# Optimization experiments

Measured on AMD Instinct MI355X. Metric: run time of the kernel, lower is better.

## Reference

```python
import jax, jax.numpy as jnp
import numpy as np

WIRES = 4
LAYERS = 2
FEAT = 16

_CNOT = jnp.array([[1, 0, 0, 0], [0, 1, 0, 0], [0, 0, 0, 1], [0, 0, 1, 0]], dtype=jnp.complex64)


def _ry(t):
    c = jnp.cos(t / 2).astype(jnp.complex64)
    s = jnp.sin(t / 2).astype(jnp.complex64)
    return jnp.stack([jnp.stack([c, -s], -1), jnp.stack([s, c], -1)], -2)


def _rx(t):
    c = jnp.cos(t / 2).astype(jnp.complex64)
    s = (-1j) * jnp.sin(t / 2).astype(jnp.complex64)
    return jnp.stack([jnp.stack([c, s], -1), jnp.stack([s, c], -1)], -2)


def _rz(t):
    e = jnp.exp(-0.5j * t.astype(jnp.complex64))
    z = jnp.zeros_like(e)
    return jnp.stack([jnp.stack([e, z], -1), jnp.stack([z, jnp.conj(e)], -1)], -2)


def _apply1(state, U, q):
    # state: (B, 2,...,2); U: (B,2,2) per-sample or (2,2) shared
    state = jnp.moveaxis(state, 1 + q, -1)
    if U.ndim == 3:
        state = jnp.einsum('b...i,bji->b...j', state, U)
    else:
        state = jnp.einsum('...i,ji->...j', state, U)
    return jnp.moveaxis(state, -1, 1 + q)


def _apply2(state, U, c, t):
    state = jnp.moveaxis(state, (1 + c, 1 + t), (-2, -1))
    shp = state.shape
    state = jnp.einsum('...i,ji->...j', state.reshape(shp[:-2] + (4,)), U).reshape(shp)
    return jnp.moveaxis(state, (-2, -1), (1 + c, 1 + t))


def _circuit(a1, a2, w):
    # a1, a2: (B, WIRES) embedding angles; w: (LAYERS, 3*WIRES) ansatz weights
    B = a1.shape[0]
    state = jnp.zeros((B,) + (2,) * WIRES, jnp.complex64).at[(slice(None),) + (0,) * WIRES].set(1.0)
    for q in range(WIRES):  # AngleEmbedding rotation='Y'
        state = _apply1(state, _ry(a1[:, q]), q)
    for q in range(WIRES):  # AngleEmbedding rotation='Z'
        state = _apply1(state, _rz(a2[:, q]), q)
    for l in range(LAYERS):
        for i in range(WIRES):
            state = _apply2(state, _CNOT, i, (i + 1) % WIRES)
        for i in range(WIRES):
            state = _apply2(state, _CNOT, i, (i + 2) % WIRES)
        for i in range(WIRES):
            state = _apply1(state, _rx(w[l, 3 * i + 0]), i)
            state = _apply1(state, _ry(w[l, 3 * i + 1]), i)
            state = _apply1(state, _rz(w[l, 3 * i + 2]), i)
    probs = state.real ** 2 + state.imag ** 2  # (B, 2,...,2)
    evs = []
    for q in range(WIRES):  # expval of PauliZ on each wire
        p = jnp.moveaxis(probs, 1 + q, 1).reshape(B, 2, -1).sum(-1)
        evs.append(p[:, 0] - p[:, 1])
    return jnp.stack(evs, -1)  # (B, WIRES)


def _qlayer(w, Xf):
    a = Xf[:, :WIRES]  # first `wires` features feed the angle embedding
    return _circuit(jnp.arctan(a), jnp.arctan(a * a), w)


def _forward(x, phi, Wd, bd):
    B, T, F = x.shape

    def step(carry, x_t):
        c, h = carry
        z = jnp.concatenate([x_t, h], -1) @ Wd + bd
        Xf = 2.0 * jax.nn.sigmoid(z) - 1.0
        f = jax.nn.sigmoid(_qlayer(phi[0], Xf))
        i = jax.nn.sigmoid(_qlayer(phi[1], Xf))
        Cg = jax.nn.sigmoid(_qlayer(phi[2], Xf))
        o = jax.nn.sigmoid(_qlayer(phi[3], Xf))
        c_new = f * c + i * Cg
        resc = o * jnp.tanh(c_new)
        h_new = _qlayer(phi[4], resc)
        y = _qlayer(phi[5], resc)
        return (c_new, h_new), y

    step = jax.checkpoint(step)
    c0 = jnp.zeros((B, WIRES), x.dtype)
    (c, h), ys = jax.lax.scan(step, (c0, c0), jnp.swapaxes(x, 0, 1))
    return jnp.swapaxes(ys, 0, 1), c, h  # (B,T,WIRES), (B,WIRES), (B,WIRES)


def setup_inputs() -> dict:
    key = jax.random.key(0)
    k1, k2, k3 = jax.random.split(key, 3)
    B, T, F = 4096, 128, FEAT
    D = F + WIRES
    return {
        'x': jax.random.normal(k1, (B, T, F), jnp.float32),
        'phi': 0.001 * jax.random.normal(k2, (6, LAYERS, 3 * WIRES), jnp.float32),
        'Wd': jax.random.normal(k3, (D, D), jnp.float32) / np.float32(np.sqrt(D)),
        'bd': jnp.zeros((D,), jnp.float32),
    }


def reference(x, phi, Wd, bd):
    return _forward(x, phi, Wd, bd)
```

## Files before the change

kernel.cpp:

```cpp
#include <hip/hip_runtime.h>
#include <math.h>

#define TSTEPS 128
#define NFEAT 16
#define NELEM 16

typedef __fp16 f16;
typedef __fp16 f16x2 __attribute__((ext_vector_type(2)));
typedef __fp16 f16x8 __attribute__((ext_vector_type(8)));
typedef float f32x2 __attribute__((ext_vector_type(2)));
typedef float f32x4 __attribute__((ext_vector_type(4)));

union F8 { f16x8 v; f16x2 h[4]; };

__device__ __forceinline__ float frcp(float x){ return __builtin_amdgcn_rcpf(x); }
__device__ __forceinline__ float frsq(float x){ return __builtin_amdgcn_rsqf(x); }
__device__ __forceinline__ float bperm(int addr, float v){
    return __int_as_float(__builtin_amdgcn_ds_bpermute(addr, __float_as_int(v)));
}
__device__ __forceinline__ f16x2 pkrtz(float a, float b){
    return __builtin_amdgcn_cvt_pkrtz(a, b);
}
__device__ __forceinline__ float dpp_xor1(float v){
    return __int_as_float(__builtin_amdgcn_update_dpp(0, __float_as_int(v), 0xB1, 0xF, 0xF, true));
}
__device__ __forceinline__ float dpp_xor2(float v){
    return __int_as_float(__builtin_amdgcn_update_dpp(0, __float_as_int(v), 0x4E, 0xF, 0xF, true));
}
__device__ __forceinline__ float swz_xor4(float v){
    return __int_as_float(__builtin_amdgcn_ds_swizzle(__float_as_int(v), 0x101F));
}
__device__ __forceinline__ float swz_xor8(float v){
    return __int_as_float(__builtin_amdgcn_ds_swizzle(__float_as_int(v), 0x201F));
}
template<int MASK> __device__ __forceinline__ float pshfl(float v){
    if constexpr (MASK == 1) return dpp_xor1(v);
    else if constexpr (MASK == 2) return dpp_xor2(v);
    else if constexpr (MASK == 4) return swz_xor4(v);
    else return swz_xor8(v);
}
__device__ __forceinline__ void cfence(){ __asm__ __volatile__("" ::: "memory"); }

__device__ __forceinline__ float sigm(float x){ return frcp(1.f + __expf(-x)); }
__device__ __forceinline__ float tanh_f(float x){ return 1.f - 2.f * frcp(__expf(2.f*x) + 1.f); }

__device__ __forceinline__ f32x2 cmul(f32x2 a, f32x2 b){
    f32x2 bs = {b.y, b.x};
    f32x2 ar = {a.x, a.x};
    f32x2 ai = {-a.y, a.y};
    return ar*b + ai*bs;
}

template<int I>
__device__ __forceinline__ void gate_step(float &re, float &im,
                                          const float* gt, int ai, int loff){
    const float4 g = *(const float4*)((const char*)gt + ai + loff);
    float pre = pshfl<(1 << I)>(re);
    float pim = pshfl<(1 << I)>(im);
    float nre = g.x*re - g.y*im + g.z*pre - g.w*pim;
    float nim = g.x*im + g.y*re + g.z*pim + g.w*pre;
    re = nre; im = nim;
}

__device__ __forceinline__ void factors(float u, float &F0r, float &F0i,
                                        float &F1r, float &F1i){
    float u2  = u * u;
    float ca1 = frsq(1.f + u2);
    float ca2 = frsq(1.f + u2*u2);
    float x1  = (1.f + ca1) * 0.5f;
    float x2  = (1.f + ca2) * 0.5f;
    float x12 = x1 * x2;
    float t   = frsq(x12);
    float a1  = u  * ca1 * 0.5f;
    float a2  = u2 * ca2 * 0.5f;
    F0r = x12 * t;
    F0i = -(a2 * x1 * t);
    F1r = a1 * x2 * t;
    F1i = a1 * a2 * t;
}

__device__ __forceinline__ void write_F(float* bc, int e, int s,
                                        float F0r, float F0i, float F1r, float F1i){
    float4 w;
    w.x = F0r; w.y = F0i; w.z = F1r; w.w = F1i;
    *(float4*)(bc + e*20 + s*4) = w;
}

__device__ __forceinline__ void build_psi(const float* bc, int e, int sm1, int sm2,
                                          F8 &bp){
    const float4 w0 = *(const float4*)(bc + e*20);
    const float4 w1 = *(const float4*)(bc + e*20 + 4);
    const f32x2 F2 = *(const f32x2*)(bc + e*20 + 8  + sm1*2);
    const f32x2 F3 = *(const f32x2*)(bc + e*20 + 12 + sm2*2);
    f32x2 w00 = {w0.x, w0.y}, w01 = {w0.z, w0.w};
    f32x2 w10 = {w1.x, w1.y}, w11 = {w1.z, w1.w};
    f32x2 pre = cmul(F2, F3);
    f32x2 P0 = cmul(pre, w10);
    f32x2 P1 = cmul(pre, w11);
    f32x2 a0 = cmul(P0, w00);
    f32x2 a1 = cmul(P0, w01);
    f32x2 a2 = cmul(P1, w00);
    f32x2 a3 = cmul(P1, w01);
    bp.h[0] = pkrtz(a0.x, a0.y);
    bp.h[1] = pkrtz(a1.x, a1.y);
    bp.h[2] = pkrtz(a2.x, a2.y);
    bp.h[3] = pkrtz(a3.x, a3.y);
}

__device__ __forceinline__ F8 pack_P(const f32x4 &reE, const f32x4 &imE,
                                     const f32x4 &reO, const f32x4 &imO){
    f32x4 pE = reE*reE + imE*imE;
    f32x4 pO = reO*reO + imO*imO;
    F8 b;
    b.h[0] = pkrtz(pE[0], pE[1]);
    b.h[1] = pkrtz(pE[2], pE[3]);
    b.h[2] = pkrtz(pO[0], pO[1]);
    b.h[3] = pkrtz(pO[2], pO[3]);
    return b;
}

__device__ __forceinline__ float sel4(float a0, float a1, float a2, float a3, int s){
    float lo = (s & 1) ? a1 : a0;
    float hi = (s & 1) ? a3 : a2;
    return (s & 2) ? hi : lo;
}

__global__ void __launch_bounds__(64, 1) qlstm_kernel(
    const float* __restrict__ x, const float* __restrict__ phi,
    const float* __restrict__ Wd, const float* __restrict__ bd,
    float* __restrict__ out, int B)
{
    __shared__ __align__(16) float gtab[384];
    __shared__ __align__(16) float ldsf[3072];
    const int UBo = 0;
    const int BCo = 0;

    const int tid  = threadIdx.x;
    const int lane = tid & 63;
    const int m    = lane & 15;
    const int grp  = lane >> 4;

    for (int idx = tid; idx < 96; idx += 64){
        int i = idx & 3, l = (idx >> 2) & 1, bb = (idx >> 3) & 1, k = idx >> 4;
        const float* pp = phi + (k*2 + l)*12 + 3*i;
        float ca, sa, cb, sb, cg, sg;
        __sincosf(0.5f*pp[0], &sa, &ca);
        __sincosf(0.5f*pp[1], &sb, &cb);
        __sincosf(0.5f*pp[2], &sg, &cg);
        float Ar, Ai, Br, Bi;
        if (bb == 0){
            float m00r = cb*ca,  m00i = sb*sa;
            float m01r = -sb*ca, m01i = -cb*sa;
            Ar = m00r*cg + m00i*sg;  Ai = m00i*cg - m00r*sg;
            Br = m01r*cg + m01i*sg;  Bi = m01i*cg - m01r*sg;
        } else {
            float m10r = sb*ca, m10i = -cb*sa;
            float m11r = cb*ca, m11i = -sb*sa;
            Ar = m11r*cg - m11i*sg;  Ai = m11i*cg + m11r*sg;
            Br = m10r*cg - m10i*sg;  Bi = m10i*cg + m10r*sg;
        }
        float* dst = gtab + (l*4 + i)*48 + (k*2 + bb)*4;
        dst[0] = Ar; dst[1] = Ai; dst[2] = Br; dst[3] = Bi;
    }
    __syncthreads();

    const int n0 = m & 1, n1 = (m >> 1) & 1, n2 = (m >> 2) & 1, n3 = (m >> 3) & 1;
    const int pm = (n0^n1^n2) | ((n0^n2^n3) << 1) | ((n0^n1^n3) << 2) | ((n0^n1) << 3);
    const int bpaddr = ((lane & 48) | pm) * 4;

    for (int k = 0; k < 6; ++k){
        int ga0 = 0*192 + k*32 + ((m >> 0) & 1)*16;
        int ga1 = 1*192 + k*32 + ((m >> 1) & 1)*16;
        int ga2 = 2*192 + k*32 + ((m >> 2) & 1)*16;
        int ga3 = 3*192 + k*32 + ((m >> 3) & 1)*16;
        for (int cb = 0; cb < 4; ++cb){
            int c = cb*4 + grp;
            float re = (pm == c) ? 1.f : 0.f;
            float im = 0.f;
            gate_step<0>(re, im, gtab, ga0, 0);   gate_step<1>(re, im, gtab, ga1, 0);
            gate_step<2>(re, im, gtab, ga2, 0);   gate_step<3>(re, im, gtab, ga3, 0);
            re = bperm(bpaddr, re);
            im = bperm(bpaddr, im);
            gate_step<0>(re, im, gtab, ga0, 768); gate_step<1>(re, im, gtab, ga1, 768);
            gate_step<2>(re, im, gtab, ga2, 768); gate_step<3>(re, im, gtab, ga3, 768);
            float2* dst = (float2*)&ldsf[UBo + k*512 + m*32 + c*2];
            *dst = make_float2(re, im);
        }
    }
    __syncthreads();

    const int e = lane & 15;
    const int s = lane >> 4;
    const int sm1 = s & 1, sm2 = s >> 1;
    const int ecol = e & 3;

    F8 are[6], aim[6];
    #pragma unroll
    for (int k = 0; k < 6; ++k){
        const float* ub = &ldsf[UBo + k*512 + e*32 + s*8];
        float4 u01 = *(const float4*)ub;
        float4 u23 = *(const float4*)(ub + 4);
        are[k].h[0] = (f16x2){(f16)u01.x, (f16)(-u01.y)};
        are[k].h[1] = (f16x2){(f16)u01.z, (f16)(-u01.w)};
        are[k].h[2] = (f16x2){(f16)u23.x, (f16)(-u23.y)};
        are[k].h[3] = (f16x2){(f16)u23.z, (f16)(-u23.w)};
        aim[k].h[0] = (f16x2){(f16)u01.y, (f16)u01.x};
        aim[k].h[1] = (f16x2){(f16)u01.w, (f16)u01.z};
        aim[k].h[2] = (f16x2){(f16)u23.y, (f16)u23.x};
        aim[k].h[3] = (f16x2){(f16)u23.w, (f16)u23.z};
    }
    __syncthreads();

    F8 asig;
    {
        int q = e >> 2;
        bool evenrows = (e & 3) < 2;
        #pragma unroll
        for (int j = 0; j < 8; ++j){
            int amp = 4*s + (j & 3);
            float v = 0.f;
            if (evenrows == (j < 4))
                v = ((amp >> q) & 1) ? -1.f : 1.f;
            asig.v[j] = (f16)v;
        }
    }
    F8 asigF, asigI;
    #pragma unroll
    for (int u = 0; u < 8; ++u){
        int amp = 4*s + (u & 3);
        float sg = ((amp >> ecol) & 1) ? -1.f : 1.f;
        asigF.v[u] = (f16)(u < 4 ? sg : 0.f);
        asigI.v[u] = (f16)(u >= 4 ? sg : 0.f);
    }

    F8 az;
    #pragma unroll
    for (int j = 0; j < 4; ++j){
        int k0 = s*8 + 2*j, k1 = k0 + 1;
        float v0 = (k0 < 16) ? Wd[k0*20 + (e >> 2)] : 0.f;
        float v1 = (k1 < 16) ? Wd[k1*20 + (e >> 2)] : 0.f;
        az.h[j] = (f16x2){(f16)v0, (f16)v1};
    }
    const float bdv = bd[s];
    const float4 wqs = make_float4(Wd[16*20 + s], Wd[17*20 + s],
                                   Wd[18*20 + s], Wd[19*20 + s]);

    const int b0 = blockIdx.x * NELEM;
    const float* xp = x + (size_t)(b0 + e) * TSTEPS * NFEAT;
    const float* xq = (s < 2) ? (xp + s*8) : xp;
    float* yp = out + (size_t)(b0 + e) * TSTEPS * 4 + s;

    const f32x4 z4 = {0.f, 0.f, 0.f, 0.f};
    float cst = 0.f;
    f32x4 hv = z4;

    float4 xa = *(const float4*)(xq);
    float4 xb = *(const float4*)(xq + 4);
    F8 bz;
    bz.h[0] = pkrtz(xa.x, xa.y);
    bz.h[1] = pkrtz(xa.z, xa.w);
    bz.h[2] = pkrtz(xb.x, xb.y);
    bz.h[3] = pkrtz(xb.z, xb.w);
    f32x4 dzx = __builtin_amdgcn_mfma_f32_16x16x32_f16(az.v, bz.v, z4, 0, 0, 0);
    xa = *(const float4*)(xq + NFEAT);
    xb = *(const float4*)(xq + NFEAT + 4);

    #pragma clang loop unroll(disable)
    for (int t = 0; t < TSTEPS; ++t){
        float zval = dzx[0] + bdv
                   + wqs.x*hv[0] + wqs.y*hv[1] + wqs.z*hv[2] + wqs.w*hv[3];
        float usel = 1.f - 2.f*frcp(__expf(zval) + 1.f);
        float F0r, F0i, F1r, F1i;
        factors(usel, F0r, F0i, F1r, F1i);
        write_F(&ldsf[BCo], e, s, F0r, F0i, F1r, F1i);
        cfence();
        F8 bp;
        build_psi(&ldsf[BCo], e, sm1, sm2, bp);

        f32x4 dre[4], dim4[4];
        #pragma unroll
        for (int k = 0; k < 4; ++k){
            dre[k]  = __builtin_amdgcn_mfma_f32_16x16x32_f16(are[k].v, bp.v, z4, 0,0,0);
            dim4[k] = __builtin_amdgcn_mfma_f32_16x16x32_f16(aim[k].v, bp.v, z4, 0,0,0);
        }
        F8 pb1 = pack_P(dre[0], dim4[0], dre[1], dim4[1]);
        F8 pb2 = pack_P(dre[2], dim4[2], dre[3], dim4[3]);
        f32x4 ev1 = __builtin_amdgcn_mfma_f32_16x16x32_f16(asig.v, pb1.v, z4, 0,0,0);
        f32x4 ev2 = __builtin_amdgcn_mfma_f32_16x16x32_f16(asig.v, pb2.v, z4, 0,0,0);

        if (t + 1 < TSTEPS){
            bz.h[0] = pkrtz(xa.x, xa.y);
            bz.h[1] = pkrtz(xa.z, xa.w);
            bz.h[2] = pkrtz(xb.x, xb.y);
            bz.h[3] = pkrtz(xb.z, xb.w);
            dzx = __builtin_amdgcn_mfma_f32_16x16x32_f16(az.v, bz.v, z4, 0,0,0);
            if (t + 2 < TSTEPS){
                xa = *(const float4*)(xq + (t+2)*NFEAT);
                xb = *(const float4*)(xq + (t+2)*NFEAT + 4);
            }
        }

        float fg = sigm(ev1[0]), ig = sigm(ev1[2]), Cg = sigm(ev2[0]), og = sigm(ev2[2]);
        cst = fg*cst + ig*Cg;
        float rs = og * tanh_f(cst);
        factors(rs, F0r, F0i, F1r, F1i);
        write_F(&ldsf[BCo], e, s, F0r, F0i, F1r, F1i);
        cfence();
        F8 bpp;
        build_psi(&ldsf[BCo], e, sm1, sm2, bpp);

        f32x4 hre = __builtin_amdgcn_mfma_f32_16x16x32_f16(are[4].v, bpp.v, z4, 0,0,0);
        f32x4 him = __builtin_amdgcn_mfma_f32_16x16x32_f16(aim[4].v, bpp.v, z4, 0,0,0);
        f32x4 yre = __builtin_amdgcn_mfma_f32_16x16x32_f16(are[5].v, bpp.v, z4, 0,0,0);
        f32x4 yim = __builtin_amdgcn_mfma_f32_16x16x32_f16(aim[5].v, bpp.v, z4, 0,0,0);
        F8 b3 = pack_P(hre, him, yre, yim);
        hv = __builtin_amdgcn_mfma_f32_16x16x32_f16(asigF.v, b3.v, z4, 0,0,0);
        f32x4 evY = __builtin_amdgcn_mfma_f32_16x16x32_f16(asigI.v, b3.v, z4, 0,0,0);

        yp[t*4] = sel4(evY[0], evY[1], evY[2], evY[3], s);
    }

    size_t cbase = (size_t)B * TSTEPS * 4;
    out[cbase + (size_t)(b0 + e)*4 + s] = cst;
    out[cbase + (size_t)B*4 + (size_t)(b0 + e)*4 + s] = sel4(hv[0], hv[1], hv[2], hv[3], s);
}

extern "C" void kernel_launch(void* const* d_in, const int* in_sizes, int n_in,
                              void* d_out, int out_size, void* d_ws, size_t ws_size,
                              hipStream_t stream) {
    const float* x   = (const float*)d_in[0];
    const float* phi = (const float*)d_in[1];
    const float* Wd  = (const float*)d_in[2];
    const float* bd  = (const float*)d_in[3];
    float* out = (float*)d_out;
    int B = in_sizes[0] / (TSTEPS * NFEAT);
    int blocks = B / NELEM;
    hipLaunchKernelGGL(qlstm_kernel, dim3(blocks), dim3(64), 0, stream,
                       x, phi, Wd, bd, out, B);
}
```

Before: 109.8 us.

## Interleave two independent 16-sample batches per wavefront to hide recurrence latency

Each 64-thread block now processes two groups of 16 batch elements (A and B) in the same time loop, with separate LDS scratch regions for each group's state factors. The two independent recurrences are interleaved so MFMA, transcendental and LDS latencies of one chain can overlap with the other, and the grid is halved. This exposes instruction-level parallelism in a latency-bound serial scan, at the cost of more registers and half as many wavefronts to fill the GPU (128 blocks for B=4096).

```diff
diff --git a/kernel.cpp b/kernel.cpp
--- a/kernel.cpp
+++ b/kernel.cpp
@@ -3,7 +3,6 @@
 
 #define TSTEPS 128
 #define NFEAT 16
-#define NELEM 16
 
 typedef __fp16 f16;
 typedef __fp16 f16x2 __attribute__((ext_vector_type(2)));
@@ -132,8 +131,8 @@
 {
     __shared__ __align__(16) float gtab[384];
     __shared__ __align__(16) float ldsf[3072];
-    const int UBo = 0;
-    const int BCo = 0;
+    const int BCa = 0;
+    const int BCb = 512;
 
     const int tid  = threadIdx.x;
     const int lane = tid & 63;
@@ -183,7 +182,7 @@
             im = bperm(bpaddr, im);
             gate_step<0>(re, im, gtab, ga0, 768); gate_step<1>(re, im, gtab, ga1, 768);
             gate_step<2>(re, im, gtab, ga2, 768); gate_step<3>(re, im, gtab, ga3, 768);
-            float2* dst = (float2*)&ldsf[UBo + k*512 + m*32 + c*2];
+            float2* dst = (float2*)&ldsf[k*512 + m*32 + c*2];
             *dst = make_float2(re, im);
         }
     }
@@ -197,7 +196,7 @@
     F8 are[6], aim[6];
     #pragma unroll
     for (int k = 0; k < 6; ++k){
-        const float* ub = &ldsf[UBo + k*512 + e*32 + s*8];
+        const float* ub = &ldsf[k*512 + e*32 + s*8];
         float4 u01 = *(const float4*)ub;
         float4 u23 = *(const float4*)(ub + 4);
         are[k].h[0] = (f16x2){(f16)u01.x, (f16)(-u01.y)};
@@ -232,7 +231,6 @@
         asigF.v[u] = (f16)(u < 4 ? sg : 0.f);
         asigI.v[u] = (f16)(u >= 4 ? sg : 0.f);
     }
-
     F8 az;
     #pragma unroll
     for (int j = 0; j < 4; ++j){
@@ -245,84 +243,126 @@
     const float4 wqs = make_float4(Wd[16*20 + s], Wd[17*20 + s],
                                    Wd[18*20 + s], Wd[19*20 + s]);
 
-    const int b0 = blockIdx.x * NELEM;
-    const float* xp = x + (size_t)(b0 + e) * TSTEPS * NFEAT;
-    const float* xq = (s < 2) ? (xp + s*8) : xp;
-    float* yp = out + (size_t)(b0 + e) * TSTEPS * 4 + s;
+    const int b0 = blockIdx.x * 32;
+    const float* xpA = x + (size_t)(b0 + e) * TSTEPS * NFEAT;
+    const float* xpB = x + (size_t)(b0 + 16 + e) * TSTEPS * NFEAT;
+    const float* xqA = (s < 2) ? (xpA + s*8) : xpA;
+    const float* xqB = (s < 2) ? (xpB + s*8) : xpB;
+    float* ypA = out + (size_t)(b0 + e) * TSTEPS * 4 + s;
+    float* ypB = out + (size_t)(b0 + 16 + e) * TSTEPS * 4 + s;
 
     const f32x4 z4 = {0.f, 0.f, 0.f, 0.f};
-    float cst = 0.f;
-    f32x4 hv = z4;
-
-    float4 xa = *(const float4*)(xq);
-    float4 xb = *(const float4*)(xq + 4);
-    F8 bz;
-    bz.h[0] = pkrtz(xa.x, xa.y);
-    bz.h[1] = pkrtz(xa.z, xa.w);
-    bz.h[2] = pkrtz(xb.x, xb.y);
-    bz.h[3] = pkrtz(xb.z, xb.w);
-    f32x4 dzx = __builtin_amdgcn_mfma_f32_16x16x32_f16(az.v, bz.v, z4, 0, 0, 0);
-    xa = *(const float4*)(xq + NFEAT);
-    xb = *(const float4*)(xq + NFEAT + 4);
+    float cstA = 0.f, cstB = 0.f;
+    f32x4 hvA = z4, hvB = z4;
+
+    float4 xaA = *(const float4*)(xqA);
+    float4 xbA = *(const float4*)(xqA + 4);
+    float4 xaB = *(const float4*)(xqB);
+    float4 xbB = *(const float4*)(xqB + 4);
+    F8 bzA, bzB;
+    bzA.h[0] = pkrtz(xaA.x, xaA.y); bzA.h[1] = pkrtz(xaA.z, xaA.w);
+    bzA.h[2] = pkrtz(xbA.x, xbA.y); bzA.h[3] = pkrtz(xbA.z, xbA.w);
+    bzB.h[0] = pkrtz(xaB.x, xaB.y); bzB.h[1] = pkrtz(xaB.z, xaB.w);
+    bzB.h[2] = pkrtz(xbB.x, xbB.y); bzB.h[3] = pkrtz(xbB.z, xbB.w);
+    f32x4 dzxA = __builtin_amdgcn_mfma_f32_16x16x32_f16(az.v, bzA.v, z4, 0,0,0);
+    f32x4 dzxB = __builtin_amdgcn_mfma_f32_16x16x32_f16(az.v, bzB.v, z4, 0,0,0);
+    xaA = *(const float4*)(xqA + NFEAT);
+    xbA = *(const float4*)(xqA + NFEAT + 4);
+    xaB = *(const float4*)(xqB + NFEAT);
+    xbB = *(const float4*)(xqB + NFEAT + 4);
 
     #pragma clang loop unroll(disable)
     for (int t = 0; t < TSTEPS; ++t){
-        float zval = dzx[0] + bdv
-                   + wqs.x*hv[0] + wqs.y*hv[1] + wqs.z*hv[2] + wqs.w*hv[3];
-        float usel = 1.f - 2.f*frcp(__expf(zval) + 1.f);
-        float F0r, F0i, F1r, F1i;
-        factors(usel, F0r, F0i, F1r, F1i);
-        write_F(&ldsf[BCo], e, s, F0r, F0i, F1r, F1i);
+        float zvalA = dzxA[0] + bdv
+                    + wqs.x*hvA[0] + wqs.y*hvA[1] + wqs.z*hvA[2] + wqs.w*hvA[3];
+        float zvalB = dzxB[0] + bdv
+                    + wqs.x*hvB[0] + wqs.y*hvB[1] + wqs.z*hvB[2] + wqs.w*hvB[3];
+        float uselA = 1.f - 2.f*frcp(__expf(zvalA) + 1.f);
+        float uselB = 1.f - 2.f*frcp(__expf(zvalB) + 1.f);
+        float FA0r, FA0i, FA1r, FA1i, FB0r, FB0i, FB1r, FB1i;
+        factors(uselA, FA0r, FA0i, FA1r, FA1i);
+        factors(uselB, FB0r, FB0i, FB1r, FB1i);
+        write_F(&ldsf[BCa], e, s, FA0r, FA0i, FA1r, FA1i);
+        write_F(&ldsf[BCb], e, s, FB0r, FB0i, FB1r, FB1i);
         cfence();
-        F8 bp;
-        build_psi(&ldsf[BCo], e, sm1, sm2, bp);
-
-        f32x4 dre[4], dim4[4];
+        F8 bpA, bpB;
+        build_psi(&ldsf[BCa], e, sm1, sm2, bpA);
+        build_psi(&ldsf[BCb], e, sm1, sm2, bpB);
+
+        f32x4 dreA[4], dimA[4], dreB[4], dimB[4];
         #pragma unroll
         for (int k = 0; k < 4; ++k){
-            dre[k]  = __builtin_amdgcn_mfma_f32_16x16x32_f16(are[k].v, bp.v, z4, 0,0,0);
-            dim4[k] = __builtin_amdgcn_mfma_f32_16x16x32_f16(aim[k].v, bp.v, z4, 0,0,0);
-        }
-        F8 pb1 = pack_P(dre[0], dim4[0], dre[1], dim4[1]);
-        F8 pb2 = pack_P(dre[2], dim4[2], dre[3], dim4[3]);
-        f32x4 ev1 = __builtin_amdgcn_mfma_f32_16x16x32_f16(asig.v, pb1.v, z4, 0,0,0);
-        f32x4 ev2 = __builtin_amdgcn_mfma_f32_16x16x32_f16(asig.v, pb2.v, z4, 0,0,0);
+            dreA[k] = __builtin_amdgcn_mfma_f32_16x16x32_f16(are[k].v, bpA.v, z4, 0,0,0);
+            dimA[k] = __builtin_amdgcn_mfma_f32_16x16x32_f16(aim[k].v, bpA.v, z4, 0,0,0);
+        }
+        #pragma unroll
+        for (int k = 0; k < 4; ++k){
+            dreB[k] = __builtin_amdgcn_mfma_f32_16x16x32_f16(are[k].v, bpB.v, z4, 0,0,0);
+            dimB[k] = __builtin_amdgcn_mfma_f32_16x16x32_f16(aim[k].v, bpB.v, z4, 0,0,0);
+        }
+        F8 pb1A = pack_P(dreA[0], dimA[0], dreA[1], dimA[1]);
+        F8 pb2A = pack_P(dreA[2], dimA[2], dreA[3], dimA[3]);
+        F8 pb1B = pack_P(dreB[0], dimB[0], dreB[1], dimB[1]);
+        F8 pb2B = pack_P(dreB[2], dimB[2], dreB[3], dimB[3]);
+        f32x4 ev1A = __builtin_amdgcn_mfma_f32_16x16x32_f16(asig.v, pb1A.v, z4, 0,0,0);
+        f32x4 ev2A = __builtin_amdgcn_mfma_f32_16x16x32_f16(asig.v, pb2A.v, z4, 0,0,0);
+        f32x4 ev1B = __builtin_amdgcn_mfma_f32_16x16x32_f16(asig.v, pb1B.v, z4, 0,0,0);
+        f32x4 ev2B = __builtin_amdgcn_mfma_f32_16x16x32_f16(asig.v, pb2B.v, z4, 0,0,0);
 
         if (t + 1 < TSTEPS){
-            bz.h[0] = pkrtz(xa.x, xa.y);
-            bz.h[1] = pkrtz(xa.z, xa.w);
-            bz.h[2] = pkrtz(xb.x, xb.y);
-            bz.h[3] = pkrtz(xb.z, xb.w);
-            dzx = __builtin_amdgcn_mfma_f32_16x16x32_f16(az.v, bz.v, z4, 0,0,0);
+            bzA.h[0] = pkrtz(xaA.x, xaA.y); bzA.h[1] = pkrtz(xaA.z, xaA.w);
+            bzA.h[2] = pkrtz(xbA.x, xbA.y); bzA.h[3] = pkrtz(xbA.z, xbA.w);
+            bzB.h[0] = pkrtz(xaB.x, xaB.y); bzB.h[1] = pkrtz(xaB.z, xaB.w);
+            bzB.h[2] = pkrtz(xbB.x, xbB.y); bzB.h[3] = pkrtz(xbB.z, xbB.w);
+            dzxA = __builtin_amdgcn_mfma_f32_16x16x32_f16(az.v, bzA.v, z4, 0,0,0);
+            dzxB = __builtin_amdgcn_mfma_f32_16x16x32_f16(az.v, bzB.v, z4, 0,0,0);
             if (t + 2 < TSTEPS){
-                xa = *(const float4*)(xq + (t+2)*NFEAT);
-                xb = *(const float4*)(xq + (t+2)*NFEAT + 4);
+                xaA = *(const float4*)(xqA + (t+2)*NFEAT);
+                xbA = *(const float4*)(xqA + (t+2)*NFEAT + 4);
+                xaB = *(const float4*)(xqB + (t+2)*NFEAT);
+                xbB = *(const float4*)(xqB + (t+2)*NFEAT + 4);
             }
         }
 
-        float fg = sigm(ev1[0]), ig = sigm(ev1[2]), Cg = sigm(ev2[0]), og = sigm(ev2[2]);
-        cst = fg*cst + ig*Cg;
-        float rs = og * tanh_f(cst);
-        factors(rs, F0r, F0i, F1r, F1i);
-        write_F(&ldsf[BCo], e, s, F0r, F0i, F1r, F1i);
+        float fgA = sigm(ev1A[0]), igA = sigm(ev1A[2]), CgA = sigm(ev2A[0]), ogA = sigm(ev2A[2]);
+        float fgB = sigm(ev1B[0]), igB = sigm(ev1B[2]), CgB = sigm(ev2B[0]), ogB = sigm(ev2B[2]);
+        cstA = fgA*cstA + igA*CgA;
+        cstB = fgB*cstB + igB*CgB;
+        float rsA = ogA * tanh_f(cstA);
+        float rsB = ogB * tanh_f(cstB);
+        factors(rsA, FA0r, FA0i, FA1r, FA1i);
+        factors(rsB, FB0r, FB0i, FB1r, FB1i);
+        write_F(&ldsf[BCa], e, s, FA0r, FA0i, FA1r, FA1i);
+        write_F(&ldsf[BCb], e, s, FB0r, FB0i, FB1r, FB1i);
         cfence();
-        F8 bpp;
-        build_psi(&ldsf[BCo], e, sm1, sm2, bpp);
-
-        f32x4 hre = __builtin_amdgcn_mfma_f32_16x16x32_f16(are[4].v, bpp.v, z4, 0,0,0);
-        f32x4 him = __builtin_amdgcn_mfma_f32_16x16x32_f16(aim[4].v, bpp.v, z4, 0,0,0);
-        f32x4 yre = __builtin_amdgcn_mfma_f32_16x16x32_f16(are[5].v, bpp.v, z4, 0,0,0);
-        f32x4 yim = __builtin_amdgcn_mfma_f32_16x16x32_f16(aim[5].v, bpp.v, z4, 0,0,0);
-        F8 b3 = pack_P(hre, him, yre, yim);
-        hv = __builtin_amdgcn_mfma_f32_16x16x32_f16(asigF.v, b3.v, z4, 0,0,0);
-        f32x4 evY = __builtin_amdgcn_mfma_f32_16x16x32_f16(asigI.v, b3.v, z4, 0,0,0);
-
-        yp[t*4] = sel4(evY[0], evY[1], evY[2], evY[3], s);
+        F8 bppA, bppB;
+        build_psi(&ldsf[BCa], e, sm1, sm2, bppA);
+        build_psi(&ldsf[BCb], e, sm1, sm2, bppB);
+
+        f32x4 hreA = __builtin_amdgcn_mfma_f32_16x16x32_f16(are[4].v, bppA.v, z4, 0,0,0);
+        f32x4 himA = __builtin_amdgcn_mfma_f32_16x16x32_f16(aim[4].v, bppA.v, z4, 0,0,0);
+        f32x4 yreA = __builtin_amdgcn_mfma_f32_16x16x32_f16(are[5].v, bppA.v, z4, 0,0,0);
+        f32x4 yimA = __builtin_amdgcn_mfma_f32_16x16x32_f16(aim[5].v, bppA.v, z4, 0,0,0);
+        f32x4 hreB = __builtin_amdgcn_mfma_f32_16x16x32_f16(are[4].v, bppB.v, z4, 0,0,0);
+        f32x4 himB = __builtin_amdgcn_mfma_f32_16x16x32_f16(aim[4].v, bppB.v, z4, 0,0,0);
+        f32x4 yreB = __builtin_amdgcn_mfma_f32_16x16x32_f16(are[5].v, bppB.v, z4, 0,0,0);
+        f32x4 yimB = __builtin_amdgcn_mfma_f32_16x16x32_f16(aim[5].v, bppB.v, z4, 0,0,0);
+        F8 b3A = pack_P(hreA, himA, yreA, yimA);
+        F8 b3B = pack_P(hreB, himB, yreB, yimB);
+        hvA = __builtin_amdgcn_mfma_f32_16x16x32_f16(asigF.v, b3A.v, z4, 0,0,0);
+        hvB = __builtin_amdgcn_mfma_f32_16x16x32_f16(asigF.v, b3B.v, z4, 0,0,0);
+        f32x4 evYA = __builtin_amdgcn_mfma_f32_16x16x32_f16(asigI.v, b3A.v, z4, 0,0,0);
+        f32x4 evYB = __builtin_amdgcn_mfma_f32_16x16x32_f16(asigI.v, b3B.v, z4, 0,0,0);
+
+        ypA[t*4] = sel4(evYA[0], evYA[1], evYA[2], evYA[3], s);
+        ypB[t*4] = sel4(evYB[0], evYB[1], evYB[2], evYB[3], s);
     }
 
     size_t cbase = (size_t)B * TSTEPS * 4;
-    out[cbase + (size_t)(b0 + e)*4 + s] = cst;
-    out[cbase + (size_t)B*4 + (size_t)(b0 + e)*4 + s] = sel4(hv[0], hv[1], hv[2], hv[3], s);
+    out[cbase + (size_t)(b0 + e)*4 + s] = cstA;
+    out[cbase + (size_t)(b0 + 16 + e)*4 + s] = cstB;
+    out[cbase + (size_t)B*4 + (size_t)(b0 + e)*4 + s] = sel4(hvA[0], hvA[1], hvA[2], hvA[3], s);
+    out[cbase + (size_t)B*4 + (size_t)(b0 + 16 + e)*4 + s] = sel4(hvB[0], hvB[1], hvB[2], hvB[3], s);
 }
 
 extern "C" void kernel_launch(void* const* d_in, const int* in_sizes, int n_in,
@@ -334,7 +374,7 @@
     const float* bd  = (const float*)d_in[3];
     float* out = (float*)d_out;
     int B = in_sizes[0] / (TSTEPS * NFEAT);
-    int blocks = B / NELEM;
+    int blocks = B / 32;
     hipLaunchKernelGGL(qlstm_kernel, dim3(blocks), dim3(64), 0, stream,
                        x, phi, Wd, bd, out, B);
 }
```

Measured after the change: 203.2 us. 85.1% more time.
